# Optimization experiments

Hardware: AMD Instinct MI355X
Metric: run time of the kernel (lower is better)

The kernel has to match this reference:

```python
import jax, jax.numpy as jnp
import numpy as np


def _conv2d_same(x, w, b):
    # x: [B,H,W,Cin], w: [kh,kw,Cin,Cout] (Keras HWIO), b: [Cout]
    y = jax.lax.conv_general_dilated(
        x, w, window_strides=(1, 1), padding='SAME',
        dimension_numbers=('NHWC', 'HWIO', 'NHWC'))
    return y + b


def _bilateral_slice_apply(grid, guide, image):
    # HDRNet bilateral_slice_apply with has_offset=True.
    # grid:  [B, gh, gw, gd, (ci+1)*co]
    # guide: [B, H, W] in [0,1]
    # image: [B, H, W, ci]
    B, gh, gw, gd, nc = grid.shape
    _, H, W, ci = image.shape
    co = nc // (ci + 1)
    dt = grid.dtype

    # Continuous grid coordinates (HDRNet convention: pixel centers, -0.5 shift)
    gx = (jnp.arange(W, dtype=dt) + 0.5) * gw / W - 0.5          # [W]
    gy = (jnp.arange(H, dtype=dt) + 0.5) * gh / H - 0.5          # [H]
    gz = guide.astype(dt) * gd - 0.5                             # [B,H,W]

    fx = jnp.floor(gx)
    fy = jnp.floor(gy)
    fz = jnp.floor(gz)
    bidx = jnp.arange(B)[:, None, None]                          # [B,1,1]

    coeffs = jnp.zeros((B, H, W, nc), dtype=dt)
    for dz in (0, 1):
        zz = fz + dz
        wz = jnp.maximum(1.0 - jnp.abs(gz - zz), 0.0)            # [B,H,W]
        zi = jnp.clip(zz.astype(jnp.int32), 0, gd - 1)           # [B,H,W]
        for dy in (0, 1):
            yy = fy + dy
            wy = jnp.maximum(1.0 - jnp.abs(gy - yy), 0.0)        # [H]
            yi = jnp.clip(yy.astype(jnp.int32), 0, gh - 1)       # [H]
            for dx in (0, 1):
                xx = fx + dx
                wx = jnp.maximum(1.0 - jnp.abs(gx - xx), 0.0)    # [W]
                xi = jnp.clip(xx.astype(jnp.int32), 0, gw - 1)   # [W]
                corner = grid[bidx, yi[None, :, None], xi[None, None, :], zi]  # [B,H,W,nc]
                w = wz * wy[None, :, None] * wx[None, None, :]   # [B,H,W]
                coeffs = coeffs + corner * w[..., None]

    # Per-pixel affine transform: coeffs -> [B,H,W,co,ci+1]
    A = coeffs.reshape(B, H, W, co, ci + 1)
    return jnp.einsum('bhwoi,bhwi->bhwo', A[..., :ci], image) + A[..., ci]


def setup_inputs() -> dict:
    key = jax.random.key(0)
    k1, k2, k3, k4 = jax.random.split(key, 4)
    B, H, W = 4, 1024, 1024
    grid = jax.random.normal(k1, (B, 16, 16, 8, 12), dtype=jnp.float32)
    guide = jax.random.uniform(k2, (B, H, W), dtype=jnp.float32)
    image = jax.random.normal(k3, (B, H, W, 3), dtype=jnp.float32)
    conv_w = jax.random.normal(k4, (3, 3, 3, 3), dtype=jnp.float32) * 0.1
    conv_b = jnp.zeros((3,), dtype=jnp.float32)
    return {'grid': grid, 'guide': guide, 'image': image,
            'conv_w': conv_w, 'conv_b': conv_b}


def reference(grid, guide, image, conv_w, conv_b):
    x = _conv2d_same(image, conv_w, conv_b)
    return _bilateral_slice_apply(grid, guide, x)
```

## Files before the change

kernel.cpp:

```cpp
#include <hip/hip_runtime.h>

#define H_  1024
#define W_  1024
#define B_  4
#define GH  16
#define GW  16
#define GD  8
#define NC  12
#define CELLF (GD * NC)
#define YROWF (GW * CELLF)

#define TW 64
#define TH 16
#define LROWS (TH + 2)
#define LCOLS (TW + 2)
#define TABF (3 * CELLF)

__device__ __forceinline__ float4 wsum4(float m0, const float4 a,
                                        float m1, const float4 b,
                                        float m2, const float4 c,
                                        float m3, const float4 d) {
    float4 r;
    r.x = m0 * a.x + m1 * b.x + m2 * c.x + m3 * d.x;
    r.y = m0 * a.y + m1 * b.y + m2 * c.y + m3 * d.y;
    r.z = m0 * a.z + m1 * b.z + m2 * c.z + m3 * d.z;
    r.w = m0 * a.w + m1 * b.w + m2 * c.w + m3 * d.w;
    return r;
}

__global__ __launch_bounds__(256)
void fused_conv_slice(const float* __restrict__ grid,
                      const float* __restrict__ guide,
                      const float* __restrict__ image,
                      const float* __restrict__ conv_w,
                      const float* __restrict__ conv_b,
                      float* __restrict__ out)
{
    __shared__ float4 s_img4[LROWS][LCOLS];
    __shared__ __align__(16) float s_tab[TH][TABF];

    const int tx  = threadIdx.x;
    const int tyq = threadIdx.y;
    const int bx  = blockIdx.x;
    const int by  = blockIdx.y;
    const int b   = blockIdx.z;
    const int x0 = bx * TW;
    const int y0 = by * TH;
    const int tid = tyq * 64 + tx;
    const int imgbase = b * (H_ * W_ * 3);

    auto stage_px = [&](int rr, int c) {
        int yy = y0 - 1 + rr;
        int xx = x0 - 1 + c;
        float4 v = make_float4(0.f, 0.f, 0.f, 0.f);
        if (yy >= 0 && yy < H_ && xx >= 0 && xx < W_) {
            const float* p = image + imgbase + (yy * W_ + xx) * 3;
            v.x = p[0]; v.y = p[1]; v.z = p[2];
        }
        s_img4[rr][c] = v;
    };
    #pragma unroll
    for (int rr0 = 0; rr0 < LROWS; rr0 += 4) {
        int rr = rr0 + tyq;
        if (rr < LROWS) {
            stage_px(rr, tx);
            if (tx < 2) stage_px(rr, TW + tx);
        }
    }

    int cells[3];
    cells[0] = max(bx - 1, 0);
    cells[1] = bx;
    cells[2] = min(bx + 1, GW - 1);
    const float* gB = grid + b * (GH * GW * GD * NC);
    {
        int rr = tid >> 4;
        int le = tid & 15;
        int y  = y0 + rr;
        float gyf = (y + 0.5f) * (1.0f / 64.0f) - 0.5f;
        float fyf = floorf(gyf);
        float tyw = gyf - fyf;
        int iy = (int)fyf;
        int yi0 = min(max(iy, 0), GH - 1);
        int yi1 = min(max(iy + 1, 0), GH - 1);
        float wy0 = 1.0f - tyw, wy1 = tyw;
        const float2* G0 = (const float2*)(gB + yi0 * YROWF);
        const float2* G1 = (const float2*)(gB + yi1 * YROWF);
        float2* T = (float2*)&s_tab[rr][0];
        #pragma unroll
        for (int k = 0; k < 9; ++k) {
            int e = le + k * 16;
            int s = (e >= 96) ? 2 : ((e >= 48) ? 1 : 0);
            int re = e - s * 48;
            int off = cells[s] * 48 + re;
            float2 v0 = G0[off], v1 = G1[off];
            float2 w;
            w.x = wy0 * v0.x + wy1 * v1.x;
            w.y = wy0 * v0.y + wy1 * v1.y;
            T[e] = w;
        }
    }

    const int x = x0 + tx;
    const int lr = tyq * 4;
    const int guidebase = b * (H_ * W_);
    float g4[4];
    #pragma unroll
    for (int j = 0; j < 4; ++j)
        g4[j] = guide[guidebase + (y0 + lr + j) * W_ + x];

    float wgt[81];
    #pragma unroll
    for (int i = 0; i < 81; ++i) wgt[i] = conv_w[i];
    float bias0 = conv_b[0], bias1 = conv_b[1], bias2 = conv_b[2];

    __syncthreads();

    float4 r0[3], r1[3], r2[3];
    float acc4[4][3];

    auto loadrow = [&](int r, float4* d) {
        d[0] = s_img4[r][tx];
        d[1] = s_img4[r][tx + 1];
        d[2] = s_img4[r][tx + 2];
    };
    auto conv3 = [&](const float4* ra, const float4* rb, const float4* rc, float* acc) {
        acc[0] = bias0; acc[1] = bias1; acc[2] = bias2;
        const float4* rows[3] = {ra, rb, rc};
        #pragma unroll
        for (int kh = 0; kh < 3; ++kh)
            #pragma unroll
            for (int kw = 0; kw < 3; ++kw) {
                float4 v4 = rows[kh][kw];
                float v[3] = {v4.x, v4.y, v4.z};
                #pragma unroll
                for (int ci = 0; ci < 3; ++ci) {
                    int wb = ((kh * 3 + kw) * 3 + ci) * 3;
                    acc[0] += v[ci] * wgt[wb + 0];
                    acc[1] += v[ci] * wgt[wb + 1];
                    acc[2] += v[ci] * wgt[wb + 2];
                }
            }
    };

    loadrow(lr + 0, r0); loadrow(lr + 1, r1); loadrow(lr + 2, r2);
    conv3(r0, r1, r2, acc4[0]);
    loadrow(lr + 3, r0); conv3(r1, r2, r0, acc4[1]);
    loadrow(lr + 4, r1); conv3(r2, r0, r1, acc4[2]);
    loadrow(lr + 5, r2); conv3(r0, r1, r2, acc4[3]);

    float gxf = (x + 0.5f) * (1.0f / 64.0f) - 0.5f;
    float fxf = floorf(gxf);
    float txw = gxf - fxf;
    float wxa = 1.0f - txw, wxb = txw;
    int s0 = (int)fxf - (bx - 1);

    const int outbase = b * (H_ * W_ * 3);

    #pragma unroll
    for (int j = 0; j < 4; ++j) {
        int y = y0 + lr + j;
        const float* Tw = &s_tab[lr + j][0];

        float gzf = g4[j] * 8.0f - 0.5f;
        float fzf = floorf(gzf);
        float tz = gzf - fzf;
        int iz = (int)fzf;
        int zb = min(max(iz, 0), GD - 2);
        float wA = (iz < 0) ? 1.0f : ((iz > GD - 2) ? 0.0f : (1.0f - tz));
        float wB = 1.0f - wA;

        const float4* pA = (const float4*)(Tw + (s0 * GD + zb) * NC);
        const float4* pB = pA + 24;
        float m0 = wxa * wA, m1 = wxa * wB, m2 = wxb * wA, m3 = wxb * wB;

        float4 c0 = wsum4(m0, pA[0], m1, pA[3], m2, pB[0], m3, pB[3]);
        float4 c1 = wsum4(m0, pA[1], m1, pA[4], m2, pB[1], m3, pB[4]);
        float4 c2 = wsum4(m0, pA[2], m1, pA[5], m2, pB[2], m3, pB[5]);

        float a0 = acc4[j][0], a1 = acc4[j][1], a2 = acc4[j][2];
        int oidx = outbase + (y * W_ + x) * 3;
        out[oidx + 0] = c0.x * a0 + c0.y * a1 + c0.z * a2 + c0.w;
        out[oidx + 1] = c1.x * a0 + c1.y * a1 + c1.z * a2 + c1.w;
        out[oidx + 2] = c2.x * a0 + c2.y * a1 + c2.z * a2 + c2.w;
    }
}

extern "C" void kernel_launch(void* const* d_in, const int* in_sizes, int n_in,
                              void* d_out, int out_size, void* d_ws, size_t ws_size,
                              hipStream_t stream) {
    const float* grid   = (const float*)d_in[0];
    const float* guide  = (const float*)d_in[1];
    const float* image  = (const float*)d_in[2];
    const float* conv_w = (const float*)d_in[3];
    const float* conv_b = (const float*)d_in[4];
    float* out = (float*)d_out;

    dim3 block(64, 4, 1);
    dim3 grid_dim(W_ / TW, H_ / TH, B_);
    fused_conv_slice<<<grid_dim, block, 0, stream>>>(grid, guide, image, conv_w, conv_b, out);
}
```

Before: 143.2 us.

## Halve tile height and use packed float2 FMAs for slice interpolation

Reduces the tile height from 16 to 8 rows, so each thread computes 2 output rows instead of 4 and the grid has twice as many blocks. The per-row coefficient table staging is remapped to 32 threads per row. The trilinear blend and the affine apply are rewritten with 2-wide vector FMAs, which the compiler can lower to packed FP32 instructions. Smaller tiles mean more halo rows and more table staging per output pixel, in exchange for more parallelism and fewer registers.

```diff
diff --git a/kernel.cpp b/kernel.cpp
--- a/kernel.cpp
+++ b/kernel.cpp
@@ -11,22 +11,12 @@
 #define YROWF (GW * CELLF)
 
 #define TW 64
-#define TH 16
+#define TH 8
 #define LROWS (TH + 2)
 #define LCOLS (TW + 2)
 #define TABF (3 * CELLF)
 
-__device__ __forceinline__ float4 wsum4(float m0, const float4 a,
-                                        float m1, const float4 b,
-                                        float m2, const float4 c,
-                                        float m3, const float4 d) {
-    float4 r;
-    r.x = m0 * a.x + m1 * b.x + m2 * c.x + m3 * d.x;
-    r.y = m0 * a.y + m1 * b.y + m2 * c.y + m3 * d.y;
-    r.z = m0 * a.z + m1 * b.z + m2 * c.z + m3 * d.z;
-    r.w = m0 * a.w + m1 * b.w + m2 * c.w + m3 * d.w;
-    return r;
-}
+typedef float f2 __attribute__((ext_vector_type(2)));
 
 __global__ __launch_bounds__(256)
 void fused_conv_slice(const float* __restrict__ grid,
@@ -74,8 +64,8 @@
     cells[2] = min(bx + 1, GW - 1);
     const float* gB = grid + b * (GH * GW * GD * NC);
     {
-        int rr = tid >> 4;
-        int le = tid & 15;
+        int rr = tid >> 5;
+        int le = tid & 31;
         int y  = y0 + rr;
         float gyf = (y + 0.5f) * (1.0f / 64.0f) - 0.5f;
         float fyf = floorf(gyf);
@@ -88,26 +78,28 @@
         const float2* G1 = (const float2*)(gB + yi1 * YROWF);
         float2* T = (float2*)&s_tab[rr][0];
         #pragma unroll
-        for (int k = 0; k < 9; ++k) {
-            int e = le + k * 16;
-            int s = (e >= 96) ? 2 : ((e >= 48) ? 1 : 0);
-            int re = e - s * 48;
-            int off = cells[s] * 48 + re;
-            float2 v0 = G0[off], v1 = G1[off];
-            float2 w;
-            w.x = wy0 * v0.x + wy1 * v1.x;
-            w.y = wy0 * v0.y + wy1 * v1.y;
-            T[e] = w;
+        for (int k = 0; k < 5; ++k) {
+            int e = le + k * 32;
+            if (e < 144) {
+                int s = (e >= 96) ? 2 : ((e >= 48) ? 1 : 0);
+                int re = e - s * 48;
+                int off = cells[s] * 48 + re;
+                float2 v0 = G0[off], v1 = G1[off];
+                float2 w;
+                w.x = wy0 * v0.x + wy1 * v1.x;
+                w.y = wy0 * v0.y + wy1 * v1.y;
+                T[e] = w;
+            }
         }
     }
 
     const int x = x0 + tx;
-    const int lr = tyq * 4;
+    const int lr = tyq * 2;
     const int guidebase = b * (H_ * W_);
-    float g4[4];
-    #pragma unroll
-    for (int j = 0; j < 4; ++j)
-        g4[j] = guide[guidebase + (y0 + lr + j) * W_ + x];
+    float g2[2];
+    #pragma unroll
+    for (int j = 0; j < 2; ++j)
+        g2[j] = guide[guidebase + (y0 + lr + j) * W_ + x];
 
     float wgt[81];
     #pragma unroll
@@ -117,7 +109,7 @@
     __syncthreads();
 
     float4 r0[3], r1[3], r2[3];
-    float acc4[4][3];
+    float acc2r[2][3];
 
     auto loadrow = [&](int r, float4* d) {
         d[0] = s_img4[r][tx];
@@ -144,10 +136,9 @@
     };
 
     loadrow(lr + 0, r0); loadrow(lr + 1, r1); loadrow(lr + 2, r2);
-    conv3(r0, r1, r2, acc4[0]);
-    loadrow(lr + 3, r0); conv3(r1, r2, r0, acc4[1]);
-    loadrow(lr + 4, r1); conv3(r2, r0, r1, acc4[2]);
-    loadrow(lr + 5, r2); conv3(r0, r1, r2, acc4[3]);
+    conv3(r0, r1, r2, acc2r[0]);
+    loadrow(lr + 3, r0);
+    conv3(r1, r2, r0, acc2r[1]);
 
     float gxf = (x + 0.5f) * (1.0f / 64.0f) - 0.5f;
     float fxf = floorf(gxf);
@@ -158,11 +149,11 @@
     const int outbase = b * (H_ * W_ * 3);
 
     #pragma unroll
-    for (int j = 0; j < 4; ++j) {
+    for (int j = 0; j < 2; ++j) {
         int y = y0 + lr + j;
         const float* Tw = &s_tab[lr + j][0];
 
-        float gzf = g4[j] * 8.0f - 0.5f;
+        float gzf = g2[j] * 8.0f - 0.5f;
         float fzf = floorf(gzf);
         float tz = gzf - fzf;
         int iz = (int)fzf;
@@ -173,16 +164,34 @@
         const float4* pA = (const float4*)(Tw + (s0 * GD + zb) * NC);
         const float4* pB = pA + 24;
         float m0 = wxa * wA, m1 = wxa * wB, m2 = wxb * wA, m3 = wxb * wB;
-
-        float4 c0 = wsum4(m0, pA[0], m1, pA[3], m2, pB[0], m3, pB[3]);
-        float4 c1 = wsum4(m0, pA[1], m1, pA[4], m2, pB[1], m3, pB[4]);
-        float4 c2 = wsum4(m0, pA[2], m1, pA[5], m2, pB[2], m3, pB[5]);
-
-        float a0 = acc4[j][0], a1 = acc4[j][1], a2 = acc4[j][2];
+        f2 m0v = {m0, m0}, m1v = {m1, m1}, m2v = {m2, m2}, m3v = {m3, m3};
+
+        float4 A0 = pA[0], A1 = pA[1], A2 = pA[2];
+        float4 B0 = pA[3], B1 = pA[4], B2 = pA[5];
+        float4 C0 = pB[0], C1 = pB[1], C2 = pB[2];
+        float4 D0 = pB[3], D1 = pB[4], D2 = pB[5];
+
+        f2 A[6] = {{A0.x,A0.y},{A0.z,A0.w},{A1.x,A1.y},{A1.z,A1.w},{A2.x,A2.y},{A2.z,A2.w}};
+        f2 Bv[6] = {{B0.x,B0.y},{B0.z,B0.w},{B1.x,B1.y},{B1.z,B1.w},{B2.x,B2.y},{B2.z,B2.w}};
+        f2 Cv[6] = {{C0.x,C0.y},{C0.z,C0.w},{C1.x,C1.y},{C1.z,C1.w},{C2.x,C2.y},{C2.z,C2.w}};
+        f2 Dv[6] = {{D0.x,D0.y},{D0.z,D0.w},{D1.x,D1.y},{D1.z,D1.w},{D2.x,D2.y},{D2.z,D2.w}};
+        f2 c[6];
+        #pragma unroll
+        for (int k = 0; k < 6; ++k)
+            c[k] = __builtin_elementwise_fma(A[k], m0v,
+                   __builtin_elementwise_fma(Bv[k], m1v,
+                   __builtin_elementwise_fma(Cv[k], m2v, Dv[k] * m3v)));
+
+        float a0 = acc2r[j][0], a1 = acc2r[j][1], a2 = acc2r[j][2];
+        f2 q0 = {a0, a1}, q1 = {a2, 1.0f};
+        f2 t0 = __builtin_elementwise_fma(c[0], q0, c[1] * q1);
+        f2 t1 = __builtin_elementwise_fma(c[2], q0, c[3] * q1);
+        f2 t2 = __builtin_elementwise_fma(c[4], q0, c[5] * q1);
+
         int oidx = outbase + (y * W_ + x) * 3;
-        out[oidx + 0] = c0.x * a0 + c0.y * a1 + c0.z * a2 + c0.w;
-        out[oidx + 1] = c1.x * a0 + c1.y * a1 + c1.z * a2 + c1.w;
-        out[oidx + 2] = c2.x * a0 + c2.y * a1 + c2.z * a2 + c2.w;
+        out[oidx + 0] = t0.x + t0.y;
+        out[oidx + 1] = t1.x + t1.y;
+        out[oidx + 2] = t2.x + t2.y;
     }
 }
 
```

After: 137.0 us. -4.4%, faster.
